# Kernel optimization log

Measured on AMD Instinct MI355X. Metric: run time of the kernel, lower is better.

## Reference

```python
import jax, jax.numpy as jnp
import numpy as np

DIM = 2048; S = 2048; B = 2; H = 16
Q_LORA = 1536; KV_LORA = 512
NOPE = 128; ROPE = 64; VHD = 128
QK_HD = NOPE + ROPE  # 192


def _linear_params(key, out_dim, in_dim):
    k1, k2 = jax.random.split(key)
    w = jax.random.normal(k1, (out_dim, in_dim), jnp.float32) * 0.02
    b = jax.random.normal(k2, (out_dim,), jnp.float32) * 0.02
    return w, b


def setup_inputs() -> dict:
    key = jax.random.key(0)
    ks = jax.random.split(key, 8)
    x = jax.random.normal(ks[0], (B, S, DIM), jnp.float32)
    # RoPE tables (interleaved convention, half-dim = ROPE//2)
    inv_freq = 1.0 / (10000.0 ** (jnp.arange(ROPE // 2, dtype=jnp.float32) / (ROPE // 2)))
    ang = jnp.arange(S, dtype=jnp.float32)[:, None] * inv_freq[None, :]  # [S, 32]
    freqs_cos = jnp.cos(ang)
    freqs_sin = jnp.sin(ang)
    Wq_down_w, Wq_down_b = _linear_params(ks[1], Q_LORA, DIM)
    q_norm_w = jnp.ones((Q_LORA,), jnp.float32)
    Wq_up_w, Wq_up_b = _linear_params(ks[2], H * QK_HD, Q_LORA)
    Wkv_down_w, Wkv_down_b = _linear_params(ks[3], KV_LORA + ROPE, DIM)
    kv_norm_w = jnp.ones((KV_LORA,), jnp.float32)
    Wkv_up_w, Wkv_up_b = _linear_params(ks[4], H * (NOPE + VHD), KV_LORA)
    Wo_w, Wo_b = _linear_params(ks[5], DIM, H * VHD)
    return dict(x=x, freqs_cos=freqs_cos, freqs_sin=freqs_sin,
                Wq_down_w=Wq_down_w, Wq_down_b=Wq_down_b, q_norm_w=q_norm_w,
                Wq_up_w=Wq_up_w, Wq_up_b=Wq_up_b,
                Wkv_down_w=Wkv_down_w, Wkv_down_b=Wkv_down_b, kv_norm_w=kv_norm_w,
                Wkv_up_w=Wkv_up_w, Wkv_up_b=Wkv_up_b, Wo_w=Wo_w, Wo_b=Wo_b)


def _rmsnorm(x, w):
    eps = jnp.finfo(x.dtype).eps
    var = jnp.mean(jnp.square(x), axis=-1, keepdims=True)
    return x * jax.lax.rsqrt(var + eps) * w


def _rope(x, cos, sin):
    # x: [B, S, H, D] with consecutive (real, imag) pairs; cos/sin: [S, D//2]
    xr = x[..., 0::2]
    xi = x[..., 1::2]
    c = cos[None, :, None, :]
    s = sin[None, :, None, :]
    yr = xr * c - xi * s
    yi = xr * s + xi * c
    return jnp.stack([yr, yi], axis=-1).reshape(x.shape)


def reference(x, freqs_cos, freqs_sin, Wq_down_w, Wq_down_b, q_norm_w,
              Wq_up_w, Wq_up_b, Wkv_down_w, Wkv_down_b, kv_norm_w,
              Wkv_up_w, Wkv_up_b, Wo_w, Wo_b):
    Bx, Sx, _ = x.shape
    # Q path: down-proj -> RMSNorm -> up-proj
    q_lat = _rmsnorm(x @ Wq_down_w.T + Wq_down_b, q_norm_w)
    Q = (q_lat @ Wq_up_w.T + Wq_up_b).reshape(Bx, Sx, H, QK_HD)
    Q_nope, Q_rope = Q[..., :NOPE], Q[..., NOPE:]
    Q_rope = _rope(Q_rope, freqs_cos, freqs_sin)
    Q = jnp.concatenate([Q_nope, Q_rope], axis=-1)
    # KV path
    kv = x @ Wkv_down_w.T + Wkv_down_b
    kv_lat, k_rope = kv[..., :KV_LORA], kv[..., KV_LORA:]
    kv_lat = _rmsnorm(kv_lat, kv_norm_w)
    k_rope = _rope(k_rope[:, :, None, :], freqs_cos, freqs_sin)  # [B,S,1,ROPE]
    knv = (kv_lat @ Wkv_up_w.T + Wkv_up_b).reshape(Bx, Sx, H, NOPE + VHD)
    K_nope, V = knv[..., :NOPE], knv[..., NOPE:]
    K = jnp.concatenate([K_nope, jnp.broadcast_to(k_rope, (Bx, Sx, H, ROPE))], axis=-1)
    # causal SDPA, scale = 1/sqrt(qk_head_dim)
    scale = QK_HD ** -0.5
    scores = jnp.einsum('bqhd,bkhd->bhqk', Q, K) * scale
    causal = jnp.tril(jnp.ones((Sx, Sx), bool))
    scores = jnp.where(causal[None, None], scores, jnp.finfo(scores.dtype).min)
    attn = jax.nn.softmax(scores, axis=-1)
    out = jnp.einsum('bhqk,bkhd->bqhd', attn, V).reshape(Bx, Sx, H * VHD)
    return out @ Wo_w.T + Wo_b
```

## Files before the change

### kernel.cpp

```cpp
#include <hip/hip_runtime.h>
#include <hip/hip_bf16.h>

typedef unsigned short u16;
typedef short s16x8 __attribute__((ext_vector_type(8)));
typedef short s16x4 __attribute__((ext_vector_type(4)));
typedef float f32x4 __attribute__((ext_vector_type(4)));

#define SEQ   2048
#define BATCH 2
#define NHEAD 16

__device__ __forceinline__ float b2f(u16 u) {
    unsigned x = ((unsigned)u) << 16;
    return __builtin_bit_cast(float, x);
}
__device__ __forceinline__ u16 f2b(float f) {
    unsigned x = __builtin_bit_cast(unsigned, f);
    unsigned r = (x + 0x7fffu + ((x >> 16) & 1u)) >> 16;
    return (u16)r;
}
__device__ __forceinline__ u16 f2b_hw(float f) {
    return __builtin_bit_cast(u16, __float2bfloat16(f));
}
__device__ __forceinline__ s16x8 comb(s16x4 lo, s16x4 hi) {
    return __builtin_shufflevector(lo, hi, 0, 1, 2, 3, 4, 5, 6, 7);
}
__device__ __forceinline__ void gload16(const void* g, void* l) {
    __builtin_amdgcn_global_load_lds(
        (const __attribute__((address_space(1))) void*)g,
        (__attribute__((address_space(3))) void*)l, 16, 0, 0);
}

__global__ __launch_bounds__(256) void cvt4_k(
    const float* __restrict__ x, const float* __restrict__ wqd,
    const float* __restrict__ wkvd, const float* __restrict__ wqu,
    u16* __restrict__ xb, u16* __restrict__ wqdb,
    u16* __restrict__ wkvdb, u16* __restrict__ wqub)
{
    const int total = 4358144;
    int i = blockIdx.x * 256 + threadIdx.x;
    const int stride = gridDim.x * 256;
    for (; i < total; i += stride) {
        const float4* src; ushort4* dst; int off;
        if (i < 2097152)      { src = (const float4*)x;    dst = (ushort4*)xb;    off = i; }
        else if (i < 2883584) { src = (const float4*)wqd;  dst = (ushort4*)wqdb;  off = i - 2097152; }
        else if (i < 3178496) { src = (const float4*)wkvd; dst = (ushort4*)wkvdb; off = i - 2883584; }
        else                  { src = (const float4*)wqu;  dst = (ushort4*)wqub;  off = i - 3178496; }
        float4 v = src[off];
        ushort4 o = { f2b(v.x), f2b(v.y), f2b(v.z), f2b(v.w) };
        dst[off] = o;
    }
}

__global__ __launch_bounds__(256) void cvt_bf16_k(
    const float* __restrict__ in, u16* __restrict__ out, int n4)
{
    int i = blockIdx.x * 256 + threadIdx.x;
    const int stride = gridDim.x * 256;
    for (; i < n4; i += stride) {
        float4 v = ((const float4*)in)[i];
        ushort4 o = { f2b(v.x), f2b(v.y), f2b(v.z), f2b(v.w) };
        ((ushort4*)out)[i] = o;
    }
}

template <int OUT_BF16>
__global__ __launch_bounds__(256) void gemm_bf_k(
    const u16* __restrict__ A, const u16* __restrict__ W,
    const float* __restrict__ bias, void* __restrict__ Cout,
    int M, int N, int K, int lda)
{
    __shared__ u16 lsA[128 * 64];
    __shared__ u16 lsB[128 * 64];
    const int tid  = threadIdx.x;
    const int lane = tid & 63;
    const int w    = tid >> 6;
    const int wm   = w >> 1, wn = w & 1;
    const int row0 = blockIdx.y * 128;
    const int col0 = blockIdx.x * 128;
    const int lr8  = lane >> 3;
    const int lc8  = (lane & 7) * 8;

    f32x4 acc[4][4];
#pragma unroll
    for (int i = 0; i < 4; i++)
#pragma unroll
        for (int j = 0; j < 4; j++) acc[i][j] = (f32x4){0.f, 0.f, 0.f, 0.f};

    for (int kt = 0; kt < K; kt += 64) {
#pragma unroll
        for (int t = 0; t < 4; t++) {
            const int r = w * 32 + t * 8;
            gload16(A + (size_t)(row0 + r + lr8) * lda + kt + lc8, &lsA[r * 64]);
            int rw = col0 + r + lr8; if (rw >= N) rw = N - 1;
            gload16(W + (size_t)rw * K + kt + lc8, &lsB[r * 64]);
        }
        __syncthreads();
#pragma unroll
        for (int ks = 0; ks < 2; ks++) {
            const int ko = ks * 32 + (lane >> 4) * 8;
            s16x8 af[4], bfr[4];
#pragma unroll
            for (int i = 0; i < 4; i++) {
                af[i]  = *(const s16x8*)&lsA[(wm * 64 + i * 16 + (lane & 15)) * 64 + ko];
                bfr[i] = *(const s16x8*)&lsB[(wn * 64 + i * 16 + (lane & 15)) * 64 + ko];
            }
#pragma unroll
            for (int mf = 0; mf < 4; mf++)
#pragma unroll
                for (int nf = 0; nf < 4; nf++)
                    acc[mf][nf] = __builtin_amdgcn_mfma_f32_16x16x32_bf16(
                        af[mf], bfr[nf], acc[mf][nf], 0, 0, 0);
        }
        __syncthreads();
    }

    const int rb = row0 + wm * 64 + ((lane >> 4) << 2);
    const int cb = col0 + wn * 64 + (lane & 15);
#pragma unroll
    for (int nf = 0; nf < 4; nf++) {
        const int col = cb + nf * 16;
        if (col < N) {
            const float bv = bias[col];
#pragma unroll
            for (int mf = 0; mf < 4; mf++)
#pragma unroll
                for (int r = 0; r < 4; r++) {
                    const int row = rb + mf * 16 + r;
                    float v = acc[mf][nf][r] + bv;
                    if (OUT_BF16) ((u16*)Cout)[(size_t)row * N + col] = f2b(v);
                    else          ((float*)Cout)[(size_t)row * N + col] = v;
                }
        }
    }
}

__global__ __launch_bounds__(256) void gemm_qup_k(
    const u16* __restrict__ A, const u16* __restrict__ W,
    const float* __restrict__ bias, u16* __restrict__ Cout,
    const float* __restrict__ fc, const float* __restrict__ fs)
{
    __shared__ u16 lsA[128 * 64];
    __shared__ u16 lsB[128 * 64];
    const int tid  = threadIdx.x;
    const int lane = tid & 63;
    const int w    = tid >> 6;
    const int wm   = w >> 1, wn = w & 1;
    const int row0 = blockIdx.y * 128;
    const int col0 = blockIdx.x * 128;
    const int lr8  = lane >> 3;
    const int lc8  = (lane & 7) * 8;
    const float QS = 0.10411754f;

    f32x4 acc[4][4];
#pragma unroll
    for (int i = 0; i < 4; i++)
#pragma unroll
        for (int j = 0; j < 4; j++) acc[i][j] = (f32x4){0.f, 0.f, 0.f, 0.f};

    for (int kt = 0; kt < 1536; kt += 64) {
#pragma unroll
        for (int t = 0; t < 4; t++) {
            const int r = w * 32 + t * 8;
            gload16(A + (size_t)(row0 + r + lr8) * 1536 + kt + lc8, &lsA[r * 64]);
            gload16(W + (size_t)(col0 + r + lr8) * 1536 + kt + lc8, &lsB[r * 64]);
        }
        __syncthreads();
#pragma unroll
        for (int ks = 0; ks < 2; ks++) {
            const int ko = ks * 32 + (lane >> 4) * 8;
            s16x8 af[4], bfr[4];
#pragma unroll
            for (int i = 0; i < 4; i++) {
                af[i]  = *(const s16x8*)&lsA[(wm * 64 + i * 16 + (lane & 15)) * 64 + ko];
                bfr[i] = *(const s16x8*)&lsB[(wn * 64 + i * 16 + (lane & 15)) * 64 + ko];
            }
#pragma unroll
            for (int mf = 0; mf < 4; mf++)
#pragma unroll
                for (int nf = 0; nf < 4; nf++)
                    acc[mf][nf] = __builtin_amdgcn_mfma_f32_16x16x32_bf16(
                        af[mf], bfr[nf], acc[mf][nf], 0, 0, 0);
        }
        __syncthreads();
    }

    const int rb = row0 + wm * 64 + ((lane >> 4) << 2);
    const int cb = col0 + wn * 64 + (lane & 15);
#pragma unroll
    for (int nf = 0; nf < 4; nf++) {
        const int col = cb + nf * 16;
        const float bv = bias[col];
        const int colBase = col0 + wn * 64 + nf * 16;
        const int dh0 = colBase % 192;
        const bool ropeBlk = (dh0 >= 128);
        const int ib = (dh0 - 128 + (lane & 15)) >> 1;
#pragma unroll
        for (int mf = 0; mf < 4; mf++)
#pragma unroll
            for (int r = 0; r < 4; r++) {
                const int row = rb + mf * 16 + r;
                float v = acc[mf][nf][r] + bv;
                if (ropeBlk) {
                    const float pp = __shfl_xor(v, 1);
                    const int s = row & (SEQ - 1);
                    const float c = fc[s * 32 + ib], sn = fs[s * 32 + ib];
                    v = (lane & 1) ? (v * c + pp * sn) : (v * c - pp * sn);
                }
                Cout[(size_t)row * 3072 + col] = f2b(v * QS);
            }
    }
}

__global__ __launch_bounds__(256) void gemm_down_k(
    const u16* __restrict__ A, const u16* __restrict__ W0,
    const u16* __restrict__ W1, const float* __restrict__ b0,
    const float* __restrict__ b1, u16* __restrict__ C0, u16* __restrict__ C1)
{
    __shared__ u16 lsA[128 * 64];
    __shared__ u16 lsB[128 * 64];
    const int tid  = threadIdx.x;
    const int lane = tid & 63;
    const int w    = tid >> 6;
    const int wm   = w >> 1, wn = w & 1;
    const int row0 = blockIdx.y * 128;
    const int col0 = blockIdx.x * 128;
    const int lr8  = lane >> 3;
    const int lc8  = (lane & 7) * 8;
    const bool in1 = (col0 >= 1536);
    const u16* Wm  = in1 ? W1 : W0;
    const int wbase = in1 ? col0 - 1536 : col0;
    const int wmax  = in1 ? 575 : 1535;

    f32x4 acc[4][4];
#pragma unroll
    for (int i = 0; i < 4; i++)
#pragma unroll
        for (int j = 0; j < 4; j++) acc[i][j] = (f32x4){0.f, 0.f, 0.f, 0.f};

    for (int kt = 0; kt < 2048; kt += 64) {
#pragma unroll
        for (int t = 0; t < 4; t++) {
            const int r = w * 32 + t * 8;
            gload16(A + (size_t)(row0 + r + lr8) * 2048 + kt + lc8, &lsA[r * 64]);
            int rw = wbase + r + lr8; if (rw > wmax) rw = wmax;
            gload16(Wm + (size_t)rw * 2048 + kt + lc8, &lsB[r * 64]);
        }
        __syncthreads();
#pragma unroll
        for (int ks = 0; ks < 2; ks++) {
            const int ko = ks * 32 + (lane >> 4) * 8;
            s16x8 af[4], bfr[4];
#pragma unroll
            for (int i = 0; i < 4; i++) {
                af[i]  = *(const s16x8*)&lsA[(wm * 64 + i * 16 + (lane & 15)) * 64 + ko];
                bfr[i] = *(const s16x8*)&lsB[(wn * 64 + i * 16 + (lane & 15)) * 64 + ko];
            }
#pragma unroll
            for (int mf = 0; mf < 4; mf++)
#pragma unroll
                for (int nf = 0; nf < 4; nf++)
                    acc[mf][nf] = __builtin_amdgcn_mfma_f32_16x16x32_bf16(
                        af[mf], bfr[nf], acc[mf][nf], 0, 0, 0);
        }
        __syncthreads();
    }

    const int rb = row0 + wm * 64 + ((lane >> 4) << 2);
    const int cb = col0 + wn * 64 + (lane & 15);
#pragma unroll
    for (int nf = 0; nf < 4; nf++) {
        const int col = cb + nf * 16;
        if (col < 2112) {
            const bool c1 = (col >= 1536);
            const float bv = c1 ? b1[col - 1536] : b0[col];
#pragma unroll
            for (int mf = 0; mf < 4; mf++)
#pragma unroll
                for (int r = 0; r < 4; r++) {
                    const int row = rb + mf * 16 + r;
                    float v = acc[mf][nf][r] + bv;
                    if (c1) C1[(size_t)row * 576 + col - 1536] = f2b(v);
                    else    C0[(size_t)row * 1536 + col] = f2b(v);
                }
        }
    }
}

__global__ __launch_bounds__(256) void norm_rope_k(
    u16* __restrict__ qlat, u16* __restrict__ kvb,
    const float* __restrict__ qnw, const float* __restrict__ kvnw,
    const float* __restrict__ fc, const float* __restrict__ fs,
    u16* __restrict__ krope)
{
    const int bid = blockIdx.x;
    const int row = bid & 4095;
    const bool isq = bid < 4096;
    u16* xr = isq ? qlat + (size_t)row * 1536 : kvb + (size_t)row * 576;
    const int cols = isq ? 1536 : 512;
    const float* wv = isq ? qnw : kvnw;

    if (!isq && threadIdx.x < 32) {
        const int i = threadIdx.x;
        const int s = row & (SEQ - 1);
        const u16* src = kvb + (size_t)row * 576 + 512 + 2 * i;
        const float xr0 = b2f(src[0]), xi0 = b2f(src[1]);
        const float c = fc[s * 32 + i], sn = fs[s * 32 + i];
        ushort2 o;
        o.x = f2b(xr0 * c - xi0 * sn);
        o.y = f2b(xr0 * sn + xi0 * c);
        *((ushort2*)(krope + (size_t)row * 64) + i) = o;
    }

    float ss = 0.f;
    for (int c = threadIdx.x; c < cols; c += 256) { float v = b2f(xr[c]); ss += v * v; }
#pragma unroll
    for (int off = 32; off; off >>= 1) ss += __shfl_xor(ss, off);
    __shared__ float red[4];
    if ((threadIdx.x & 63) == 0) red[threadIdx.x >> 6] = ss;
    __syncthreads();
    const float tot = red[0] + red[1] + red[2] + red[3];
    const float inv = rsqrtf(tot / (float)cols + 1.1920929e-7f);
    for (int c = threadIdx.x; c < cols; c += 256)
        xr[c] = f2b(b2f(xr[c]) * inv * wv[c]);
}

__global__ __launch_bounds__(256, 2) void attn_k(
    const u16* __restrict__ Q, const u16* __restrict__ KNV,
    const u16* __restrict__ KR, u16* __restrict__ O)
{
    __shared__ u16 k_lds[64][200];
    __shared__ u16 v_t[128][68];

    const int tid  = threadIdx.x;
    const int lane = tid & 63;
    const int w    = tid >> 6;
    const int lr   = lane & 15;
    const int lq   = lane >> 4;

    const int bid = blockIdx.x;
    const int qt  = (bid < 256) ? (15 - (bid >> 5)) : ((bid - 256) >> 5);
    const int bh  = bid & 31;
    const int h   = bh & 15;
    const int b   = bh >> 4;
    const int q0  = qt * 128;
    const int bS  = b * SEQ;

    s16x8 qf[2][6];
#pragma unroll
    for (int mb = 0; mb < 2; mb++) {
        const u16* qp = Q + (size_t)(bS + q0 + w * 32 + mb * 16 + lr) * 3072
                        + h * 192 + (lq << 2);
#pragma unroll
        for (int kc = 0; kc < 6; kc++)
            qf[mb][kc] = comb(*(const s16x4*)(qp + kc * 32),
                              *(const s16x4*)(qp + kc * 32 + 16));
    }

    f32x4 o_acc[2][8];
#pragma unroll
    for (int mb = 0; mb < 2; mb++)
#pragma unroll
        for (int d = 0; d < 8; d++) o_acc[mb][d] = (f32x4){0.f, 0.f, 0.f, 0.f};
    float m_run[2] = { -1e30f, -1e30f };
    float l_run[2] = { 0.f, 0.f };

    const int ntiles = (q0 + 128) / 64;

    s16x8 kr[6], vr[4];
    const int kkey = tid >> 2;
    const int ka   = tid & 3;

    {
        const u16* kn  = KNV + (size_t)(bS + kkey) * 4096 + h * 256;
        const u16* krp = KR + (size_t)(bS + kkey) * 64;
#pragma unroll
        for (int i = 0; i < 6; i++) {
            const int col = ka * 48 + i * 8;
            kr[i] = *(const s16x8*)(col < 128 ? kn + col : krp + (col - 128));
        }
#pragma unroll
        for (int i = 0; i < 4; i++) {
            const int idx = tid + i * 256;
            vr[i] = *(const s16x8*)(KNV + (size_t)(bS + (idx >> 4)) * 4096
                                    + h * 256 + 128 + (idx & 15) * 8);
        }
    }

    for (int t = 0; t < ntiles; t++) {
#pragma unroll
        for (int i = 0; i < 6; i++)
            *(s16x8*)&k_lds[kkey][ka * 48 + i * 8] = kr[i];
#pragma unroll
        for (int i = 0; i < 4; i++) {
            const int idx = tid + i * 256;
            const int key = idx >> 4, d0 = (idx & 15) * 8;
            const int xw = (d0 >> 4) << 2;
#pragma unroll
            for (int e = 0; e < 8; e++) v_t[d0 + e][key ^ xw] = (u16)vr[i][e];
        }
        __syncthreads();

        if (t + 1 < ntiles) {
            const int nk = (t + 1) * 64;
            const u16* kn  = KNV + (size_t)(bS + nk + kkey) * 4096 + h * 256;
            const u16* krp = KR + (size_t)(bS + nk + kkey) * 64;
#pragma unroll
            for (int i = 0; i < 6; i++) {
                const int col = ka * 48 + i * 8;
                kr[i] = *(const s16x8*)(col < 128 ? kn + col : krp + (col - 128));
            }
#pragma unroll
            for (int i = 0; i < 4; i++) {
                const int idx = tid + i * 256;
                vr[i] = *(const s16x8*)(KNV + (size_t)(bS + nk + (idx >> 4)) * 4096
                                        + h * 256 + 128 + (idx & 15) * 8);
            }
        }

        const int kt0 = t * 64;

        f32x4 sa[2][4];
#pragma unroll
        for (int mb = 0; mb < 2; mb++)
#pragma unroll
            for (int f = 0; f < 4; f++) sa[mb][f] = (f32x4){0.f, 0.f, 0.f, 0.f};
#pragma unroll
        for (int kc = 0; kc < 6; kc++) {
            const int kb = kc * 32 + (lq << 2);
#pragma unroll
            for (int f = 0; f < 4; f++) {
                s16x8 kf = comb(*(const s16x4*)&k_lds[f * 16 + lr][kb],
                                *(const s16x4*)&k_lds[f * 16 + lr][kb + 16]);
                sa[0][f] = __builtin_amdgcn_mfma_f32_16x16x32_bf16(kf, qf[0][kc], sa[0][f], 0, 0, 0);
                sa[1][f] = __builtin_amdgcn_mfma_f32_16x16x32_bf16(kf, qf[1][kc], sa[1][f], 0, 0, 0);
            }
        }

        s16x8 pb[2][2];
#pragma unroll
        for (int mb = 0; mb < 2; mb++) {
            const int qrow = q0 + w * 32 + mb * 16 + lr;
            const bool need_mask = (kt0 + 63 > qrow);
            float p[4][4];
#pragma unroll
            for (int f = 0; f < 4; f++)
#pragma unroll
                for (int r = 0; r < 4; r++) {
                    float s = sa[mb][f][r];
                    if (need_mask && (kt0 + f * 16 + lq * 4 + r > qrow)) s = -1e30f;
                    p[f][r] = s;
                }
            float tm = p[0][0];
#pragma unroll
            for (int f = 0; f < 4; f++)
#pragma unroll
                for (int r = 0; r < 4; r++) tm = fmaxf(tm, p[f][r]);
            tm = fmaxf(tm, __shfl_xor(tm, 16));
            tm = fmaxf(tm, __shfl_xor(tm, 32));

            const float mo = m_run[mb];
            const bool keep = __all(tm <= mo + 8.f);
            float corr = 1.f;
            if (!keep) {
                const float nm = fmaxf(mo, tm);
                corr = __builtin_amdgcn_exp2f(mo - nm);
                m_run[mb] = nm;
            }
            const float mbase = m_run[mb];
#pragma unroll
            for (int f = 0; f < 4; f++)
#pragma unroll
                for (int r = 0; r < 4; r++)
                    p[f][r] = __builtin_amdgcn_exp2f(p[f][r] - mbase);
            float ps = 0.f;
#pragma unroll
            for (int f = 0; f < 4; f++)
#pragma unroll
                for (int r = 0; r < 4; r++) ps += p[f][r];
            ps += __shfl_xor(ps, 16);
            ps += __shfl_xor(ps, 32);
            l_run[mb] = l_run[mb] * corr + ps;
            if (!keep) {
#pragma unroll
                for (int d = 0; d < 8; d++)
#pragma unroll
                    for (int r = 0; r < 4; r++) o_acc[mb][d][r] *= corr;
            }
#pragma unroll
            for (int hf = 0; hf < 2; hf++) {
                s16x8 v;
#pragma unroll
                for (int j = 0; j < 8; j++)
                    v[j] = (short)f2b_hw(p[hf * 2 + (j >> 2)][j & 3]);
                pb[mb][hf] = v;
            }
        }

#pragma unroll
        for (int hf = 0; hf < 2; hf++) {
            const int pc = hf * 32 + (lq << 2);
#pragma unroll
            for (int df = 0; df < 8; df++) {
                const int row = df * 16 + lr;
                const int xr0 = df << 2;
                s16x8 vf = comb(*(const s16x4*)&v_t[row][pc ^ xr0],
                                *(const s16x4*)&v_t[row][(pc + 16) ^ xr0]);
                o_acc[0][df] = __builtin_amdgcn_mfma_f32_16x16x32_bf16(vf, pb[0][hf], o_acc[0][df], 0, 0, 0);
                o_acc[1][df] = __builtin_amdgcn_mfma_f32_16x16x32_bf16(vf, pb[1][hf], o_acc[1][df], 0, 0, 0);
            }
        }
        __syncthreads();
    }

#pragma unroll
    for (int mb = 0; mb < 2; mb++) {
        const float invl = 1.f / l_run[mb];
        u16* op = O + (size_t)(bS + q0 + w * 32 + mb * 16 + lr) * 2048 + h * 128 + lq * 4;
#pragma unroll
        for (int df = 0; df < 8; df++) {
            ushort4 ov = { f2b_hw(o_acc[mb][df][0] * invl), f2b_hw(o_acc[mb][df][1] * invl),
                           f2b_hw(o_acc[mb][df][2] * invl), f2b_hw(o_acc[mb][df][3] * invl) };
            *(ushort4*)(op + df * 16) = ov;
        }
    }
}

extern "C" void kernel_launch(void* const* d_in, const int* in_sizes, int n_in,
                              void* d_out, int out_size, void* d_ws, size_t ws_size,
                              hipStream_t stream)
{
    const float* x    = (const float*)d_in[0];
    const float* fc   = (const float*)d_in[1];
    const float* fs   = (const float*)d_in[2];
    const float* Wqd  = (const float*)d_in[3];
    const float* bqd  = (const float*)d_in[4];
    const float* qnw  = (const float*)d_in[5];
    const float* Wqu  = (const float*)d_in[6];
    const float* bqu  = (const float*)d_in[7];
    const float* Wkvd = (const float*)d_in[8];
    const float* bkvd = (const float*)d_in[9];
    const float* kvnw = (const float*)d_in[10];
    const float* Wkvu = (const float*)d_in[11];
    const float* bkvu = (const float*)d_in[12];
    const float* Wo   = (const float*)d_in[13];
    const float* bo   = (const float*)d_in[14];

    char* ws = (char*)d_ws;
    u16* kvb     = (u16*)(ws);
    u16* qlat    = (u16*)(ws + 4718592);
    u16* qbuf    = (u16*)(ws + 17301504);
    u16* krope   = (u16*)(ws + 42467328);
    u16* knv     = (u16*)(ws + 42991616);
    u16* attn_o  = (u16*)(ws);
    u16* x_bf    = (u16*)(ws + 17301504);
    u16* wqd_bf  = (u16*)(ws + 42991616);
    u16* wkvd_bf = (u16*)(ws + 49283072);
    u16* wqu_bf  = (u16*)(ws + 51642368);
    u16* wkvu_bf = (u16*)(ws + 4718592);
    u16* wo_bf   = (u16*)(ws + 42991616);

    const int M = BATCH * SEQ;

    cvt4_k<<<2048, 256, 0, stream>>>(x, Wqd, Wkvd, Wqu, x_bf, wqd_bf, wkvd_bf, wqu_bf);
    gemm_down_k<<<dim3(17, 32), 256, 0, stream>>>(x_bf, wqd_bf, wkvd_bf, bqd, bkvd, qlat, kvb);
    norm_rope_k<<<8192, 256, 0, stream>>>(qlat, kvb, qnw, kvnw, fc, fs, krope);
    gemm_qup_k<<<dim3(24, 32), 256, 0, stream>>>(qlat, wqu_bf, bqu, qbuf, fc, fs);
    cvt_bf16_k<<<1024, 256, 0, stream>>>(Wkvu, wkvu_bf, 2097152 / 4);
    gemm_bf_k<1><<<dim3(32, 32), 256, 0, stream>>>(kvb, wkvu_bf, bkvu, knv, M, 4096, 512, 576);
    attn_k<<<512, 256, 0, stream>>>(qbuf, knv, krope, attn_o);
    cvt_bf16_k<<<1024, 256, 0, stream>>>(Wo, wo_bf, 4194304 / 4);
    gemm_bf_k<0><<<dim3(16, 32), 256, 0, stream>>>(attn_o, wo_bf, bo, (float*)d_out, M, 2048, 2048, 2048);
}
```

Baseline: 410.0 us.

## Unify GEMMs into 256x256 double-buffered 8-wave kernel with swizzled LDS

Replaces the three separate 128x128 single-buffered GEMM kernels with one templated 256x256-tile, 512-thread kernel. It double-buffers LDS with async global loads issued ahead, uses XOR-swizzled LDS addressing to avoid bank conflicts, and raises MFMA priority with s_setprio. The aim is to hide global-load latency behind MFMA work and raise data reuse per tile. The trade-offs are more registers and LDS per block and fewer blocks per GEMM, which can leave CUs idle on the smaller GEMMs.

```diff
diff --git a/kernel.cpp b/kernel.cpp
--- a/kernel.cpp
+++ b/kernel.cpp
@@ -64,225 +64,217 @@
     }
 }
 
-template <int OUT_BF16>
-__global__ __launch_bounds__(256) void gemm_bf_k(
-    const u16* __restrict__ A, const u16* __restrict__ W,
-    const float* __restrict__ bias, void* __restrict__ Cout,
-    int M, int N, int K, int lda)
+template <int MODE>
+__global__ __launch_bounds__(512, 2) void gemm8p_k(
+    const u16* __restrict__ A, const u16* __restrict__ W0,
+    const u16* __restrict__ W1, const float* __restrict__ b0,
+    const float* __restrict__ b1, void* __restrict__ C0, void* __restrict__ C1,
+    int N, int K, int lda,
+    const float* __restrict__ fc, const float* __restrict__ fs)
 {
-    __shared__ u16 lsA[128 * 64];
-    __shared__ u16 lsB[128 * 64];
+    __shared__ u16 lsA[2][2][128 * 64];
+    __shared__ u16 lsB[2][2][128 * 64];
     const int tid  = threadIdx.x;
     const int lane = tid & 63;
     const int w    = tid >> 6;
-    const int wm   = w >> 1, wn = w & 1;
-    const int row0 = blockIdx.y * 128;
-    const int col0 = blockIdx.x * 128;
-    const int lr8  = lane >> 3;
-    const int lc8  = (lane & 7) * 8;
-
-    f32x4 acc[4][4];
-#pragma unroll
-    for (int i = 0; i < 4; i++)
+    const int wm   = w >> 2;
+    const int wn   = w & 3;
+    const int row0 = blockIdx.y * 256;
+    const int col0 = blockIdx.x * 256;
+    const int nt   = K / 64;
+
+    auto stageA = [&](int t, int h) {
+        const int kt = t * 64, buf = t & 1;
+#pragma unroll
+        for (int j = 0; j < 2; j++) {
+            const int g = (w * 2 + j) * 64 + lane;
+            const int row = g >> 3, c16 = g & 7;
+            const int cs = c16 ^ (row & 7);
+            gload16(A + (size_t)(row0 + h * 128 + row) * lda + kt + cs * 8,
+                    &lsA[buf][h][(w * 2 + j) * 512]);
+        }
+    };
+    auto stageB = [&](int t, int h) {
+        const int kt = t * 64, buf = t & 1;
+#pragma unroll
+        for (int j = 0; j < 2; j++) {
+            const int g = (w * 2 + j) * 64 + lane;
+            const int row = g >> 3, c16 = g & 7;
+            const int cs = c16 ^ (row & 7);
+            int rw = col0 + h * 128 + row;
+            const u16* Wp;
+            if (MODE == 3) {
+                const bool in1 = rw >= 1536;
+                int r2 = in1 ? rw - 1536 : rw;
+                if (in1 && r2 > 575) r2 = 575;
+                Wp = (in1 ? W1 : W0) + (size_t)r2 * K;
+            } else {
+                if (rw >= N) rw = N - 1;
+                Wp = W0 + (size_t)rw * K;
+            }
+            gload16(Wp + kt + cs * 8, &lsB[buf][h][(w * 2 + j) * 512]);
+        }
+    };
+    auto readA = [&](int buf, int mf, int kh) -> s16x8 {
+        const int ra = mf * 16 + (lane & 15);
+        const int c16 = kh * 4 + (lane >> 4);
+        return *(const s16x8*)&lsA[buf][wm][(ra * 8 + (c16 ^ (ra & 7))) * 8];
+    };
+    auto readB = [&](int buf, int nf, int kh) -> s16x8 {
+        const int rb = (wn & 1) * 64 + nf * 16 + (lane & 15);
+        const int c16 = kh * 4 + (lane >> 4);
+        return *(const s16x8*)&lsB[buf][wn >> 1][(rb * 8 + (c16 ^ (rb & 7))) * 8];
+    };
+
+    f32x4 acc[8][4];
+#pragma unroll
+    for (int i = 0; i < 8; i++)
 #pragma unroll
         for (int j = 0; j < 4; j++) acc[i][j] = (f32x4){0.f, 0.f, 0.f, 0.f};
 
-    for (int kt = 0; kt < K; kt += 64) {
-#pragma unroll
-        for (int t = 0; t < 4; t++) {
-            const int r = w * 32 + t * 8;
-            gload16(A + (size_t)(row0 + r + lr8) * lda + kt + lc8, &lsA[r * 64]);
-            int rw = col0 + r + lr8; if (rw >= N) rw = N - 1;
-            gload16(W + (size_t)rw * K + kt + lc8, &lsB[r * 64]);
-        }
-        __syncthreads();
-#pragma unroll
-        for (int ks = 0; ks < 2; ks++) {
-            const int ko = ks * 32 + (lane >> 4) * 8;
-            s16x8 af[4], bfr[4];
-#pragma unroll
-            for (int i = 0; i < 4; i++) {
-                af[i]  = *(const s16x8*)&lsA[(wm * 64 + i * 16 + (lane & 15)) * 64 + ko];
-                bfr[i] = *(const s16x8*)&lsB[(wn * 64 + i * 16 + (lane & 15)) * 64 + ko];
-            }
-#pragma unroll
-            for (int mf = 0; mf < 4; mf++)
-#pragma unroll
-                for (int nf = 0; nf < 4; nf++)
-                    acc[mf][nf] = __builtin_amdgcn_mfma_f32_16x16x32_bf16(
-                        af[mf], bfr[nf], acc[mf][nf], 0, 0, 0);
-        }
-        __syncthreads();
-    }
-
-    const int rb = row0 + wm * 64 + ((lane >> 4) << 2);
-    const int cb = col0 + wn * 64 + (lane & 15);
+    stageB(0, 0); stageB(0, 1); stageA(0, 0); stageA(0, 1);
+    stageB(1, 0); stageB(1, 1);
+    asm volatile("s_waitcnt vmcnt(4)" ::: "memory");
+    asm volatile("s_barrier" ::: "memory");
+
+    for (int t = 0; t < nt; t++) {
+        const int buf = t & 1;
+        s16x8 bfr[4][2];
+#pragma unroll
+        for (int nf = 0; nf < 4; nf++)
+#pragma unroll
+            for (int kh = 0; kh < 2; kh++) bfr[nf][kh] = readB(buf, nf, kh);
+        {
+            s16x8 af[2][2];
+#pragma unroll
+            for (int m2 = 0; m2 < 2; m2++)
+#pragma unroll
+                for (int kh = 0; kh < 2; kh++) af[m2][kh] = readA(buf, m2, kh);
+            if (t + 1 < nt) stageA(t + 1, 0);
+            __builtin_amdgcn_s_setprio(1);
+#pragma unroll
+            for (int kh = 0; kh < 2; kh++)
+#pragma unroll
+                for (int m2 = 0; m2 < 2; m2++)
+#pragma unroll
+                    for (int nf = 0; nf < 4; nf++)
+                        acc[m2][nf] = __builtin_amdgcn_mfma_f32_16x16x32_bf16(
+                            af[m2][kh], bfr[nf][kh], acc[m2][nf], 0, 0, 0);
+            __builtin_amdgcn_s_setprio(0);
+        }
+        asm volatile("s_barrier" ::: "memory");
+        {
+            s16x8 af[2][2];
+#pragma unroll
+            for (int m2 = 0; m2 < 2; m2++)
+#pragma unroll
+                for (int kh = 0; kh < 2; kh++) af[m2][kh] = readA(buf, 2 + m2, kh);
+            if (t + 1 < nt) stageA(t + 1, 1);
+            if (t + 2 < nt) stageB(t + 2, 0);
+            __builtin_amdgcn_s_setprio(1);
+#pragma unroll
+            for (int kh = 0; kh < 2; kh++)
+#pragma unroll
+                for (int m2 = 0; m2 < 2; m2++)
+#pragma unroll
+                    for (int nf = 0; nf < 4; nf++)
+                        acc[2 + m2][nf] = __builtin_amdgcn_mfma_f32_16x16x32_bf16(
+                            af[m2][kh], bfr[nf][kh], acc[2 + m2][nf], 0, 0, 0);
+            __builtin_amdgcn_s_setprio(0);
+        }
+        {
+            s16x8 af[2][2];
+#pragma unroll
+            for (int m2 = 0; m2 < 2; m2++)
+#pragma unroll
+                for (int kh = 0; kh < 2; kh++) af[m2][kh] = readA(buf, 4 + m2, kh);
+            if (t + 2 < nt) stageB(t + 2, 1);
+            __builtin_amdgcn_s_setprio(1);
+#pragma unroll
+            for (int kh = 0; kh < 2; kh++)
+#pragma unroll
+                for (int m2 = 0; m2 < 2; m2++)
+#pragma unroll
+                    for (int nf = 0; nf < 4; nf++)
+                        acc[4 + m2][nf] = __builtin_amdgcn_mfma_f32_16x16x32_bf16(
+                            af[m2][kh], bfr[nf][kh], acc[4 + m2][nf], 0, 0, 0);
+            __builtin_amdgcn_s_setprio(0);
+        }
+        {
+            s16x8 af[2][2];
+#pragma unroll
+            for (int m2 = 0; m2 < 2; m2++)
+#pragma unroll
+                for (int kh = 0; kh < 2; kh++) af[m2][kh] = readA(buf, 6 + m2, kh);
+            __builtin_amdgcn_s_setprio(1);
+#pragma unroll
+            for (int kh = 0; kh < 2; kh++)
+#pragma unroll
+                for (int m2 = 0; m2 < 2; m2++)
+#pragma unroll
+                    for (int nf = 0; nf < 4; nf++)
+                        acc[6 + m2][nf] = __builtin_amdgcn_mfma_f32_16x16x32_bf16(
+                            af[m2][kh], bfr[nf][kh], acc[6 + m2][nf], 0, 0, 0);
+            __builtin_amdgcn_s_setprio(0);
+        }
+        if (t + 2 < nt) asm volatile("s_waitcnt vmcnt(4)" ::: "memory");
+        else            asm volatile("s_waitcnt vmcnt(0)" ::: "memory");
+        asm volatile("s_barrier" ::: "memory");
+    }
+
+    const float QS = 0.10411754f;
+    const int rbase = row0 + wm * 128 + ((lane >> 4) << 2);
+    const int cbase = col0 + wn * 64 + (lane & 15);
 #pragma unroll
     for (int nf = 0; nf < 4; nf++) {
-        const int col = cb + nf * 16;
-        if (col < N) {
-            const float bv = bias[col];
-#pragma unroll
-            for (int mf = 0; mf < 4; mf++)
+        const int col = cbase + nf * 16;
+        if (MODE == 3) {
+            if (col < 2112) {
+                const bool c1 = col >= 1536;
+                const float bv = c1 ? b1[col - 1536] : b0[col];
+#pragma unroll
+                for (int mf = 0; mf < 8; mf++)
+#pragma unroll
+                    for (int r = 0; r < 4; r++) {
+                        const int row = rbase + mf * 16 + r;
+                        const float v = acc[mf][nf][r] + bv;
+                        if (c1) ((u16*)C1)[(size_t)row * 576 + col - 1536] = f2b_hw(v);
+                        else    ((u16*)C0)[(size_t)row * 1536 + col] = f2b_hw(v);
+                    }
+            }
+        } else if (MODE == 2) {
+            const float bv = b0[col];
+            const int colBase = col0 + wn * 64 + nf * 16;
+            const int dh0 = colBase % 192;
+            const bool ropeBlk = (dh0 >= 128);
+            const int ib = (dh0 - 128 + (lane & 15)) >> 1;
+#pragma unroll
+            for (int mf = 0; mf < 8; mf++)
 #pragma unroll
                 for (int r = 0; r < 4; r++) {
-                    const int row = rb + mf * 16 + r;
+                    const int row = rbase + mf * 16 + r;
                     float v = acc[mf][nf][r] + bv;
-                    if (OUT_BF16) ((u16*)Cout)[(size_t)row * N + col] = f2b(v);
-                    else          ((float*)Cout)[(size_t)row * N + col] = v;
+                    if (ropeBlk) {
+                        const float pp = __shfl_xor(v, 1);
+                        const int s = row & (SEQ - 1);
+                        const float c = fc[s * 32 + ib], sn = fs[s * 32 + ib];
+                        v = (lane & 1) ? (v * c + pp * sn) : (v * c - pp * sn);
+                    }
+                    ((u16*)C0)[(size_t)row * 3072 + col] = f2b_hw(v * QS);
                 }
-        }
-    }
-}
-
-__global__ __launch_bounds__(256) void gemm_qup_k(
-    const u16* __restrict__ A, const u16* __restrict__ W,
-    const float* __restrict__ bias, u16* __restrict__ Cout,
-    const float* __restrict__ fc, const float* __restrict__ fs)
-{
-    __shared__ u16 lsA[128 * 64];
-    __shared__ u16 lsB[128 * 64];
-    const int tid  = threadIdx.x;
-    const int lane = tid & 63;
-    const int w    = tid >> 6;
-    const int wm   = w >> 1, wn = w & 1;
-    const int row0 = blockIdx.y * 128;
-    const int col0 = blockIdx.x * 128;
-    const int lr8  = lane >> 3;
-    const int lc8  = (lane & 7) * 8;
-    const float QS = 0.10411754f;
-
-    f32x4 acc[4][4];
-#pragma unroll
-    for (int i = 0; i < 4; i++)
-#pragma unroll
-        for (int j = 0; j < 4; j++) acc[i][j] = (f32x4){0.f, 0.f, 0.f, 0.f};
-
-    for (int kt = 0; kt < 1536; kt += 64) {
-#pragma unroll
-        for (int t = 0; t < 4; t++) {
-            const int r = w * 32 + t * 8;
-            gload16(A + (size_t)(row0 + r + lr8) * 1536 + kt + lc8, &lsA[r * 64]);
-            gload16(W + (size_t)(col0 + r + lr8) * 1536 + kt + lc8, &lsB[r * 64]);
-        }
-        __syncthreads();
-#pragma unroll
-        for (int ks = 0; ks < 2; ks++) {
-            const int ko = ks * 32 + (lane >> 4) * 8;
-            s16x8 af[4], bfr[4];
-#pragma unroll
-            for (int i = 0; i < 4; i++) {
-                af[i]  = *(const s16x8*)&lsA[(wm * 64 + i * 16 + (lane & 15)) * 64 + ko];
-                bfr[i] = *(const s16x8*)&lsB[(wn * 64 + i * 16 + (lane & 15)) * 64 + ko];
-            }
-#pragma unroll
-            for (int mf = 0; mf < 4; mf++)
-#pragma unroll
-                for (int nf = 0; nf < 4; nf++)
-                    acc[mf][nf] = __builtin_amdgcn_mfma_f32_16x16x32_bf16(
-                        af[mf], bfr[nf], acc[mf][nf], 0, 0, 0);
-        }
-        __syncthreads();
-    }
-
-    const int rb = row0 + wm * 64 + ((lane >> 4) << 2);
-    const int cb = col0 + wn * 64 + (lane & 15);
-#pragma unroll
-    for (int nf = 0; nf < 4; nf++) {
-        const int col = cb + nf * 16;
-        const float bv = bias[col];
-        const int colBase = col0 + wn * 64 + nf * 16;
-        const int dh0 = colBase % 192;
-        const bool ropeBlk = (dh0 >= 128);
-        const int ib = (dh0 - 128 + (lane & 15)) >> 1;
-#pragma unroll
-        for (int mf = 0; mf < 4; mf++)
-#pragma unroll
-            for (int r = 0; r < 4; r++) {
-                const int row = rb + mf * 16 + r;
-                float v = acc[mf][nf][r] + bv;
-                if (ropeBlk) {
-                    const float pp = __shfl_xor(v, 1);
-                    const int s = row & (SEQ - 1);
-                    const float c = fc[s * 32 + ib], sn = fs[s * 32 + ib];
-                    v = (lane & 1) ? (v * c + pp * sn) : (v * c - pp * sn);
-                }
-                Cout[(size_t)row * 3072 + col] = f2b(v * QS);
-            }
-    }
-}
-
-__global__ __launch_bounds__(256) void gemm_down_k(
-    const u16* __restrict__ A, const u16* __restrict__ W0,
-    const u16* __restrict__ W1, const float* __restrict__ b0,
-    const float* __restrict__ b1, u16* __restrict__ C0, u16* __restrict__ C1)
-{
-    __shared__ u16 lsA[128 * 64];
-    __shared__ u16 lsB[128 * 64];
-    const int tid  = threadIdx.x;
-    const int lane = tid & 63;
-    const int w    = tid >> 6;
-    const int wm   = w >> 1, wn = w & 1;
-    const int row0 = blockIdx.y * 128;
-    const int col0 = blockIdx.x * 128;
-    const int lr8  = lane >> 3;
-    const int lc8  = (lane & 7) * 8;
-    const bool in1 = (col0 >= 1536);
-    const u16* Wm  = in1 ? W1 : W0;
-    const int wbase = in1 ? col0 - 1536 : col0;
-    const int wmax  = in1 ? 575 : 1535;
-
-    f32x4 acc[4][4];
-#pragma unroll
-    for (int i = 0; i < 4; i++)
-#pragma unroll
-        for (int j = 0; j < 4; j++) acc[i][j] = (f32x4){0.f, 0.f, 0.f, 0.f};
-
-    for (int kt = 0; kt < 2048; kt += 64) {
-#pragma unroll
-        for (int t = 0; t < 4; t++) {
-            const int r = w * 32 + t * 8;
-            gload16(A + (size_t)(row0 + r + lr8) * 2048 + kt + lc8, &lsA[r * 64]);
-            int rw = wbase + r + lr8; if (rw > wmax) rw = wmax;
-            gload16(Wm + (size_t)rw * 2048 + kt + lc8, &lsB[r * 64]);
-        }
-        __syncthreads();
-#pragma unroll
-        for (int ks = 0; ks < 2; ks++) {
-            const int ko = ks * 32 + (lane >> 4) * 8;
-            s16x8 af[4], bfr[4];
-#pragma unroll
-            for (int i = 0; i < 4; i++) {
-                af[i]  = *(const s16x8*)&lsA[(wm * 64 + i * 16 + (lane & 15)) * 64 + ko];
-                bfr[i] = *(const s16x8*)&lsB[(wn * 64 + i * 16 + (lane & 15)) * 64 + ko];
-            }
-#pragma unroll
-            for (int mf = 0; mf < 4; mf++)
-#pragma unroll
-                for (int nf = 0; nf < 4; nf++)
-                    acc[mf][nf] = __builtin_amdgcn_mfma_f32_16x16x32_bf16(
-                        af[mf], bfr[nf], acc[mf][nf], 0, 0, 0);
-        }
-        __syncthreads();
-    }
-
-    const int rb = row0 + wm * 64 + ((lane >> 4) << 2);
-    const int cb = col0 + wn * 64 + (lane & 15);
-#pragma unroll
-    for (int nf = 0; nf < 4; nf++) {
-        const int col = cb + nf * 16;
-        if (col < 2112) {
-            const bool c1 = (col >= 1536);
-            const float bv = c1 ? b1[col - 1536] : b0[col];
-#pragma unroll
-            for (int mf = 0; mf < 4; mf++)
-#pragma unroll
-                for (int r = 0; r < 4; r++) {
-                    const int row = rb + mf * 16 + r;
-                    float v = acc[mf][nf][r] + bv;
-                    if (c1) C1[(size_t)row * 576 + col - 1536] = f2b(v);
-                    else    C0[(size_t)row * 1536 + col] = f2b(v);
-                }
+        } else {
+            if (col < N) {
+                const float bv = b0[col];
+#pragma unroll
+                for (int mf = 0; mf < 8; mf++)
+#pragma unroll
+                    for (int r = 0; r < 4; r++) {
+                        const int row = rbase + mf * 16 + r;
+                        const float v = acc[mf][nf][r] + bv;
+                        if (MODE == 1) ((float*)C0)[(size_t)row * N + col] = v;
+                        else           ((u16*)C0)[(size_t)row * N + col] = f2b_hw(v);
+                    }
+            }
         }
     }
 }
@@ -560,15 +552,17 @@
     u16* wkvu_bf = (u16*)(ws + 4718592);
     u16* wo_bf   = (u16*)(ws + 42991616);
 
-    const int M = BATCH * SEQ;
-
     cvt4_k<<<2048, 256, 0, stream>>>(x, Wqd, Wkvd, Wqu, x_bf, wqd_bf, wkvd_bf, wqu_bf);
-    gemm_down_k<<<dim3(17, 32), 256, 0, stream>>>(x_bf, wqd_bf, wkvd_bf, bqd, bkvd, qlat, kvb);
+    gemm8p_k<3><<<dim3(9, 16), 512, 0, stream>>>(
+        x_bf, wqd_bf, wkvd_bf, bqd, bkvd, qlat, kvb, 2112, 2048, 2048, nullptr, nullptr);
     norm_rope_k<<<8192, 256, 0, stream>>>(qlat, kvb, qnw, kvnw, fc, fs, krope);
-    gemm_qup_k<<<dim3(24, 32), 256, 0, stream>>>(qlat, wqu_bf, bqu, qbuf, fc, fs);
+    gemm8p_k<2><<<dim3(12, 16), 512, 0, stream>>>(
+        qlat, wqu_bf, nullptr, bqu, nullptr, qbuf, nullptr, 3072, 1536, 1536, fc, fs);
     cvt_bf16_k<<<1024, 256, 0, stream>>>(Wkvu, wkvu_bf, 2097152 / 4);
-    gemm_bf_k<1><<<dim3(32, 32), 256, 0, stream>>>(kvb, wkvu_bf, bkvu, knv, M, 4096, 512, 576);
+    gemm8p_k<0><<<dim3(16, 16), 512, 0, stream>>>(
+        kvb, wkvu_bf, nullptr, bkvu, nullptr, knv, nullptr, 4096, 512, 576, nullptr, nullptr);
     attn_k<<<512, 256, 0, stream>>>(qbuf, knv, krope, attn_o);
     cvt_bf16_k<<<1024, 256, 0, stream>>>(Wo, wo_bf, 4194304 / 4);
-    gemm_bf_k<0><<<dim3(16, 32), 256, 0, stream>>>(attn_o, wo_bf, bo, (float*)d_out, M, 2048, 2048, 2048);
-}
+    gemm8p_k<1><<<dim3(8, 16), 512, 0, stream>>>(
+        attn_o, wo_bf, nullptr, bo, nullptr, d_out, nullptr, 2048, 2048, 2048, nullptr, nullptr);
+}
```

Measured after the change: 363.3 us. -11.4%, faster.
